# Optimization experiments

Measured on AMD Instinct MI355X. Metric: run time of the kernel, lower is better.

Reference implementation:

```python
import jax, jax.numpy as jnp
from jax import lax
import numpy as np

K = 3          # sampling grid size (kernel_size)
WS = 4         # scope kernel size (weight_shape)
DILATION = 1


def setup_inputs() -> dict:
    key = jax.random.key(0)
    k1, k2, k3, k4 = jax.random.split(key, 4)
    x = jax.random.normal(k1, (4, 128, 56, 56), jnp.float32)
    # offset conv is zero-initialized in the original; use small values so offsets are realistic
    offset_w = jax.random.normal(k2, (2 * K * K, 128, K, K), jnp.float32) * 0.01
    offset_b = jax.random.normal(k3, (2 * K * K,), jnp.float32) * 0.01
    weight = jax.random.normal(k4, (128, WS, WS), jnp.float32) * 0.1  # depthwise scope kernel
    return {"x": x, "offset_w": offset_w, "offset_b": offset_b, "weight": weight}


def reference(x, offset_w, offset_b, weight):
    B, C, H, W = x.shape
    K2 = K * K
    # offset conv: 3x3, stride 1, pad 1 (same geometry as main conv)
    off = lax.conv_general_dilated(
        x, offset_w, window_strides=(1, 1), padding=[(1, 1), (1, 1)],
        dimension_numbers=("NCHW", "OIHW", "NCHW"))
    off = off + offset_b[None, :, None, None]
    off = off * DILATION                     # offset_clip is None
    off = off.reshape(B, K2, 2, H, W)
    dy, dx = off[:, :, 0], off[:, :, 1]      # [B,K2,H,W]

    # base coordinates of the KxK sampling grid centered inside the WSxWS scope kernel
    base = jnp.arange(K, dtype=x.dtype) - (K - 1) / 2 + (WS - 1) / 2   # [K]
    by = jnp.repeat(base, K)                 # k = i*K + j -> row i
    bx = jnp.tile(base, K)                   # k = i*K + j -> col j
    yc = dy + by[None, :, None, None]        # [B,K2,H,W] sampling coords in kernel space
    xc = dx + bx[None, :, None, None]

    # bilinear sampling of the scope kernel (zero outside scope)
    wflat = weight.reshape(C, WS * WS)
    y0 = jnp.floor(yc)
    x0 = jnp.floor(xc)
    samp = jnp.zeros((C, B, K2, H, W), x.dtype)
    for oy, ox in ((0, 0), (0, 1), (1, 0), (1, 1)):
        yi = y0 + oy
        xi = x0 + ox
        coef = (1.0 - jnp.abs(yc - yi)) * (1.0 - jnp.abs(xc - xi))
        valid = (yi >= 0) & (yi < WS) & (xi >= 0) & (xi < WS)
        idx = (jnp.clip(yi, 0, WS - 1) * WS + jnp.clip(xi, 0, WS - 1)).astype(jnp.int32)
        vals = jnp.take(wflat, idx, axis=1)  # [C,B,K2,H,W] irregular gather
        samp = samp + (coef * valid)[None] * vals
    samp = jnp.moveaxis(samp, 0, 1)          # [B,C,K2,H,W]

    # depthwise conv with per-pixel sampled kernels (stride 1, pad 1, dilation 1)
    xp = jnp.pad(x, ((0, 0), (0, 0), (1, 1), (1, 1)))
    pats = jnp.stack([xp[:, :, i:i + H, j:j + W] for i in range(K) for j in range(K)], axis=2)
    return jnp.sum(samp * pats, axis=2)      # [B,C,H,W]
```

## Files before the change

kernel.cpp:

```cpp
#include <hip/hip_runtime.h>

#define CC 128
#define HH 56
#define WW 56
#define NK2 9
#define NO 18
#define WSZ 4
#define W64 64
#define NCG 16
#define SCG 8
#define CPG 16

#define WSA_FLOATS (224L * NCG * NO * W64)
#define WSC_ENTRIES (4L * NK2 * HH * W64)

__global__ __launch_bounds__(256) void wtrans(
    const float* __restrict__ offset_w,
    float* __restrict__ wT)
{
    const int i = blockIdx.x * 256 + threadIdx.x;
    if (i >= CC * 162) return;
    const int c = i / 162;
    int r = i - c * 162;
    const int ky = r / 54;
    const int f  = r - ky * 54;
    const int o  = f / 3, kx = f - o * 3;
    wT[c * 168 + ky * 56 + f] = offset_w[(o * CC + c) * 9 + ky * 3 + kx];
}

__global__ __launch_bounds__(256, 4) void conv_partial(
    const float* __restrict__ x,
    const float* __restrict__ wT,
    float* __restrict__ wsA)
{
    const int blk = blockIdx.x;
    const int cg  = blk & 15;
    const int bh4 = blk >> 4;
    const int b   = bh4 / 14;
    const int h4  = bh4 - b * 14;
    const int h0  = h4 * 4;
    const int t   = threadIdx.x;
    const int lane = t & 63;
    const int wv  = __builtin_amdgcn_readfirstlane(t >> 6);

    __shared__ float s_red[4][2][NO][W64];

    float acc[4][NO];
    #pragma unroll
    for (int r = 0; r < 4; ++r)
        #pragma unroll
        for (int o = 0; o < NO; ++o) acc[r][o] = 0.f;

    if (lane < WW) {
        #pragma unroll
        for (int ci = 0; ci < 2; ++ci) {
            const int c = cg * 8 + wv * 2 + ci;
            const float* xc = x + ((long)b * CC + c) * HH * WW;
            float xr[6][3];
            #pragma unroll
            for (int r6 = 0; r6 < 6; ++r6) {
                const int hy = h0 + r6 - 1;
                float v0 = 0.f, v1 = 0.f, v2 = 0.f;
                if (hy >= 0 && hy < HH) {
                    const float* row = xc + hy * WW;
                    v1 = row[lane];
                    v0 = (lane > 0)      ? row[lane - 1] : 0.f;
                    v2 = (lane < WW - 1) ? row[lane + 1] : 0.f;
                }
                xr[r6][0] = v0; xr[r6][1] = v1; xr[r6][2] = v2;
            }
            const float* wc = wT + c * 168;
            #pragma unroll
            for (int ky = 0; ky < 3; ++ky) {
                const float* wp = wc + ky * 56;
                #pragma unroll
                for (int f = 0; f < 54; ++f) {
                    const float wf = wp[f];
                    const int o = f / 3, kx = f - o * 3;
                    #pragma unroll
                    for (int r = 0; r < 4; ++r)
                        acc[r][o] += wf * xr[r + ky][kx];
                }
            }
        }
    }

    const float* sr = (const float*)s_red;
    #pragma unroll
    for (int round = 0; round < 2; ++round) {
        #pragma unroll
        for (int r2 = 0; r2 < 2; ++r2)
            #pragma unroll
            for (int o = 0; o < NO; ++o)
                s_red[wv][r2][o][lane] = acc[round * 2 + r2][o];
        __syncthreads();
        for (int s = t; s < 2 * NO * W64; s += 256) {
            const float v = sr[s] + sr[2304 + s] + sr[2 * 2304 + s] + sr[3 * 2304 + s];
            const int r2  = s / (NO * W64);
            const int rem = s - r2 * (NO * W64);
            const int bh  = b * HH + h0 + round * 2 + r2;
            wsA[((long)bh * NCG + cg) * (NO * W64) + rem] = v;
        }
        __syncthreads();
    }
}

__global__ __launch_bounds__(64) void coef_kernel(
    const float* __restrict__ wsA,
    const float* __restrict__ offset_b,
    float4* __restrict__ wsC,
    unsigned* __restrict__ wsI)
{
    const int blk = blockIdx.x;
    const int k2  = blk % NK2;
    const int bh  = blk / NK2;
    const int b   = bh / HH;
    const int h   = bh - b * HH;
    const int w   = threadIdx.x;

    const float* base = wsA + (long)bh * (NCG * NO * W64);
    float dy = offset_b[2 * k2];
    float dx = offset_b[2 * k2 + 1];
    #pragma unroll
    for (int g = 0; g < NCG; ++g) {
        dy += base[g * (NO * W64) + (2 * k2) * W64 + w];
        dx += base[g * (NO * W64) + (2 * k2 + 1) * W64 + w];
    }

    const float yc = dy + 0.5f + (float)(k2 / 3);
    const float xc = dx + 0.5f + (float)(k2 % 3);
    const float y0 = floorf(yc), x0f = floorf(xc);
    const float fy = yc - y0, fx = xc - x0f;
    const int yi = (int)y0, xi = (int)x0f;
    float cf[4]; int id[4];
    #pragma unroll
    for (int q = 0; q < 4; ++q) {
        const int oy = q >> 1, ox = q & 1;
        const int yy = yi + oy, xx = xi + ox;
        float c2 = (oy ? fy : 1.f - fy) * (ox ? fx : 1.f - fx);
        const bool valid = (yy >= 0) && (yy < WSZ) && (xx >= 0) && (xx < WSZ);
        cf[q] = valid ? c2 : 0.f;
        const int yyc = yy < 0 ? 0 : (yy > 3 ? 3 : yy);
        const int xxc = xx < 0 ? 0 : (xx > 3 ? 3 : xx);
        id[q] = yyc * 4 + xxc;
    }
    const long oidx = ((long)(b * NK2 + k2) * HH + h) * W64 + w;
    wsC[oidx] = make_float4(cf[0], cf[1], cf[2], cf[3]);
    wsI[oidx] = (unsigned)(id[0] | (id[1] << 4) | (id[2] << 8) | (id[3] << 12));
}

__global__ __launch_bounds__(256) void sample_kernel(
    const float* __restrict__ x,
    const float* __restrict__ weight,
    const float4* __restrict__ wsC,
    const unsigned* __restrict__ wsI,
    float* __restrict__ out)
{
    const int blk = blockIdx.x;
    const int bh  = blk >> 3;
    const int cg  = blk & 7;
    const int b   = bh / HH;
    const int h   = bh - b * HH;
    const int t   = threadIdx.x;
    const int lane = t & 63;
    const int wv  = __builtin_amdgcn_readfirstlane(t >> 6);

    __shared__ float s_wT[16][20];
    if (t < 256) {
        const int j = t >> 4, cl = t & 15;
        s_wT[j][cl] = weight[(cg * CPG + cl) * 16 + j];
    }
    __syncthreads();

    if (lane >= WW) return;
    const int w = lane;
    const int cl0 = wv * 4;

    float4 cf[NK2]; unsigned pk[NK2];
    const long cidx0 = ((long)b * NK2 * HH + h) * W64 + w;
    #pragma unroll
    for (int k2 = 0; k2 < NK2; ++k2) {
        cf[k2] = wsC[cidx0 + (long)k2 * HH * W64];
        pk[k2] = wsI[cidx0 + (long)k2 * HH * W64];
    }

    float xv[4][9];
    #pragma unroll
    for (int u = 0; u < 4; ++u) {
        const int c = cg * CPG + cl0 + u;
        const float* xc = x + ((long)b * CC + c) * HH * WW;
        #pragma unroll
        for (int ky = 0; ky < 3; ++ky) {
            const int hy = h + ky - 1;
            #pragma unroll
            for (int kx = 0; kx < 3; ++kx) {
                const int wx = w + kx - 1;
                float v = 0.f;
                if (hy >= 0 && hy < HH && wx >= 0 && wx < WW)
                    v = xc[hy * WW + wx];
                xv[u][ky * 3 + kx] = v;
            }
        }
    }

    float res[4] = {0.f, 0.f, 0.f, 0.f};
    #pragma unroll
    for (int k2 = 0; k2 < NK2; ++k2) {
        const unsigned p = pk[k2];
        const float4 W0 = *(const float4*)&s_wT[p & 15][cl0];
        const float4 W1 = *(const float4*)&s_wT[(p >> 4) & 15][cl0];
        const float4 W2 = *(const float4*)&s_wT[(p >> 8) & 15][cl0];
        const float4 W3 = *(const float4*)&s_wT[(p >> 12) & 15][cl0];
        const float4 c4 = cf[k2];
        res[0] += (c4.x * W0.x + c4.y * W1.x + c4.z * W2.x + c4.w * W3.x) * xv[0][k2];
        res[1] += (c4.x * W0.y + c4.y * W1.y + c4.z * W2.y + c4.w * W3.y) * xv[1][k2];
        res[2] += (c4.x * W0.z + c4.y * W1.z + c4.z * W2.z + c4.w * W3.z) * xv[2][k2];
        res[3] += (c4.x * W0.w + c4.y * W1.w + c4.z * W2.w + c4.w * W3.w) * xv[3][k2];
    }

    #pragma unroll
    for (int u = 0; u < 4; ++u) {
        const int c = cg * CPG + cl0 + u;
        out[(((long)b * CC + c) * HH + h) * WW + w] = res[u];
    }
}

extern "C" void kernel_launch(void* const* d_in, const int* in_sizes, int n_in,
                              void* d_out, int out_size, void* d_ws, size_t ws_size,
                              hipStream_t stream) {
    const float* x        = (const float*)d_in[0];
    const float* offset_w = (const float*)d_in[1];
    const float* offset_b = (const float*)d_in[2];
    const float* weight   = (const float*)d_in[3];
    float* out = (float*)d_out;

    char* p = (char*)d_ws;
    float*    wsA = (float*)p;                          p += WSA_FLOATS * 4;
    float4*   wsC = (float4*)p;                         p += WSC_ENTRIES * 16;
    unsigned* wsI = (unsigned*)p;                       p += WSC_ENTRIES * 4;
    float*    wT  = (float*)p;

    wtrans       <<<(CC * 162 + 255) / 256, 256, 0, stream>>>(offset_w, wT);
    conv_partial <<<4 * 14 * NCG, 256, 0, stream>>>(x, wT, wsA);
    coef_kernel  <<<224 * NK2, 64, 0, stream>>>(wsA, offset_b, wsC, wsI);
    sample_kernel<<<224 * SCG, 256, 0, stream>>>(x, weight, wsC, wsI, out);
}
```

Before: 97.26 us.

## Fuse offset-weight transpose into conv kernel via shared memory staging

```diff
diff --git a/kernel.cpp b/kernel.cpp
--- a/kernel.cpp
+++ b/kernel.cpp
@@ -14,23 +14,9 @@
 #define WSA_FLOATS (224L * NCG * NO * W64)
 #define WSC_ENTRIES (4L * NK2 * HH * W64)
 
-__global__ __launch_bounds__(256) void wtrans(
-    const float* __restrict__ offset_w,
-    float* __restrict__ wT)
-{
-    const int i = blockIdx.x * 256 + threadIdx.x;
-    if (i >= CC * 162) return;
-    const int c = i / 162;
-    int r = i - c * 162;
-    const int ky = r / 54;
-    const int f  = r - ky * 54;
-    const int o  = f / 3, kx = f - o * 3;
-    wT[c * 168 + ky * 56 + f] = offset_w[(o * CC + c) * 9 + ky * 3 + kx];
-}
-
 __global__ __launch_bounds__(256, 4) void conv_partial(
     const float* __restrict__ x,
-    const float* __restrict__ wT,
+    const float* __restrict__ offset_w,
     float* __restrict__ wsA)
 {
     const int blk = blockIdx.x;
@@ -43,7 +29,19 @@
     const int lane = t & 63;
     const int wv  = __builtin_amdgcn_readfirstlane(t >> 6);
 
-    __shared__ float s_red[4][2][NO][W64];
+    __shared__ float s_wt[8][168];
+    __shared__ float s_red[4][NO][W64];
+
+    const int c0 = cg * 8;
+    for (int i = t; i < NO * 72; i += 256) {
+        const int o   = i / 72;
+        const int rem = i - o * 72;
+        const int cl  = rem / 9;
+        const int j   = rem - cl * 9;
+        const int ky  = j / 3, kx = j - ky * 3;
+        s_wt[cl][ky * 56 + o * 3 + kx] = offset_w[o * (CC * 9) + (c0 + cl) * 9 + j];
+    }
+    __syncthreads();
 
     float acc[4][NO];
     #pragma unroll
@@ -54,7 +52,8 @@
     if (lane < WW) {
         #pragma unroll
         for (int ci = 0; ci < 2; ++ci) {
-            const int c = cg * 8 + wv * 2 + ci;
+            const int cl = wv * 2 + ci;
+            const int c  = c0 + cl;
             const float* xc = x + ((long)b * CC + c) * HH * WW;
             float xr[6][3];
             #pragma unroll
@@ -69,17 +68,23 @@
                 }
                 xr[r6][0] = v0; xr[r6][1] = v1; xr[r6][2] = v2;
             }
-            const float* wc = wT + c * 168;
             #pragma unroll
             for (int ky = 0; ky < 3; ++ky) {
-                const float* wp = wc + ky * 56;
+                const float4* wq = (const float4*)&s_wt[cl][ky * 56];
                 #pragma unroll
-                for (int f = 0; f < 54; ++f) {
-                    const float wf = wp[f];
-                    const int o = f / 3, kx = f - o * 3;
+                for (int q = 0; q < 14; ++q) {
+                    const float4 w4 = wq[q];
                     #pragma unroll
-                    for (int r = 0; r < 4; ++r)
-                        acc[r][o] += wf * xr[r + ky][kx];
+                    for (int e = 0; e < 4; ++e) {
+                        const int f = q * 4 + e;
+                        if (f >= 54) break;
+                        const float wf = (e == 0) ? w4.x : (e == 1) ? w4.y
+                                        : (e == 2) ? w4.z : w4.w;
+                        const int o = f / 3, kx = f - o * 3;
+                        #pragma unroll
+                        for (int r = 0; r < 4; ++r)
+                            acc[r][o] += wf * xr[r + ky][kx];
+                    }
                 }
             }
         }
@@ -87,21 +92,15 @@
 
     const float* sr = (const float*)s_red;
     #pragma unroll
-    for (int round = 0; round < 2; ++round) {
-        #pragma unroll
-        for (int r2 = 0; r2 < 2; ++r2)
-            #pragma unroll
-            for (int o = 0; o < NO; ++o)
-                s_red[wv][r2][o][lane] = acc[round * 2 + r2][o];
+    for (int round = 0; round < 4; ++round) {
         __syncthreads();
-        for (int s = t; s < 2 * NO * W64; s += 256) {
-            const float v = sr[s] + sr[2304 + s] + sr[2 * 2304 + s] + sr[3 * 2304 + s];
-            const int r2  = s / (NO * W64);
-            const int rem = s - r2 * (NO * W64);
-            const int bh  = b * HH + h0 + round * 2 + r2;
-            wsA[((long)bh * NCG + cg) * (NO * W64) + rem] = v;
-        }
+        #pragma unroll
+        for (int o = 0; o < NO; ++o) s_red[wv][o][lane] = acc[round][o];
         __syncthreads();
+        const int bh = b * HH + h0 + round;
+        float* dst = wsA + ((long)bh * NCG + cg) * (NO * W64);
+        for (int s = t; s < NO * W64; s += 256)
+            dst[s] = sr[s] + sr[1152 + s] + sr[2 * 1152 + s] + sr[3 * 1152 + s];
     }
 }
 
@@ -237,11 +236,9 @@
     char* p = (char*)d_ws;
     float*    wsA = (float*)p;                          p += WSA_FLOATS * 4;
     float4*   wsC = (float4*)p;                         p += WSC_ENTRIES * 16;
-    unsigned* wsI = (unsigned*)p;                       p += WSC_ENTRIES * 4;
-    float*    wT  = (float*)p;
-
-    wtrans       <<<(CC * 162 + 255) / 256, 256, 0, stream>>>(offset_w, wT);
-    conv_partial <<<4 * 14 * NCG, 256, 0, stream>>>(x, wT, wsA);
+    unsigned* wsI = (unsigned*)p;
+
+    conv_partial <<<4 * 14 * NCG, 256, 0, stream>>>(x, offset_w, wsA);
     coef_kernel  <<<224 * NK2, 64, 0, stream>>>(wsA, offset_b, wsC, wsI);
     sample_kernel<<<224 * SCG, 256, 0, stream>>>(x, weight, wsC, wsI, out);
 }
```

Result: slower. 133.2 us (+37.0%).
